# Kernel optimization log

Measured on AMD Instinct MI355X. Metric: run time of the kernel, lower is better.

## Reference

```python
import jax, jax.numpy as jnp
import numpy as np

H = 4            # num_attention_heads
EPS_LN = 1e-6    # LayerNorm eps
EPS_IN = 1e-5    # InstanceNorm2d eps (no affine)


def layer_norm(x, g, b):
    m = x.mean(-1, keepdims=True)
    v = ((x - m) ** 2).mean(-1, keepdims=True)
    return (x - m) * jax.lax.rsqrt(v + EPS_LN) * g + b


def instance_norm(s):
    # s: [B,H,C,KV]; InstanceNorm2d(H): normalize per (b,h) over spatial dims (C,KV)
    m = s.mean(axis=(2, 3), keepdims=True)
    v = s.var(axis=(2, 3), keepdims=True)
    return (s - m) * jax.lax.rsqrt(v + EPS_IN)


def _forward(emb1, emb2, emb3, emb4,
             an1_g, an1_b, Wq1, Wo1, fn1_g, fn1_b, fc11_w, fc11_b, fc12_w, fc12_b,
             an2_g, an2_b, Wq2, Wo2, fn2_g, fn2_b, fc21_w, fc21_b, fc22_w, fc22_b,
             an3_g, an3_b, Wq3, Wo3, fn3_g, fn3_b, fc31_w, fc31_b, fc32_w, fc32_b,
             an4_g, an4_b, Wq4, Wo4, fn4_g, fn4_b, fc41_w, fc41_b, fc42_w, fc42_b,
             anA_g, anA_b, Wk, Wv):
    embs = [emb1, emb2, emb3, emb4]
    branches = [
        (an1_g, an1_b, Wq1, Wo1, fn1_g, fn1_b, fc11_w, fc11_b, fc12_w, fc12_b),
        (an2_g, an2_b, Wq2, Wo2, fn2_g, fn2_b, fc21_w, fc21_b, fc22_w, fc22_b),
        (an3_g, an3_b, Wq3, Wo3, fn3_g, fn3_b, fc31_w, fc31_b, fc32_w, fc32_b),
        (an4_g, an4_b, Wq4, Wo4, fn4_g, fn4_b, fc41_w, fc41_b, fc42_w, fc42_b),
    ]
    emb_all = jnp.concatenate(embs, axis=-1)          # [B, n, KV]
    KV = emb_all.shape[-1]
    ea = layer_norm(emb_all, anA_g, anA_b)
    # per-head K/V projections (torch Linear: y = x @ W^T), stacked over heads
    K = jnp.einsum('bnk,hjk->bhnj', ea, Wk)           # [B,H,n,KV]
    V = jnp.einsum('bnk,hjk->bhnj', ea, Wv)           # [B,H,n,KV]
    scale = 1.0 / np.sqrt(KV).astype(np.float32)
    outs = []
    for e, (ag, ab, Wq, Wo, fg, fb, w1, b1, w2, b2) in zip(embs, branches):
        cx = layer_norm(e, ag, ab)                    # [B,n,C]
        Q = jnp.einsum('bnc,hdc->bhnd', cx, Wq)       # [B,H,n,C]
        # channel-attention scores: Q^T K over tokens -> [B,H,C,KV]
        scores = jnp.einsum('bhnd,bhnj->bhdj', Q, K) * scale
        probs = jax.nn.softmax(instance_norm(scores), axis=-1)
        # context [B,H,C,n] averaged over heads -> [B,n,C] (fused into einsum)
        ctx = jnp.einsum('bhdj,bhnj->bnd', probs, V) / H
        O = ctx @ Wo.T                                # out projection
        x = e + O                                     # residual
        h = layer_norm(x, fg, fb)
        h = jax.nn.gelu(h @ w1.T + b1, approximate=False)
        h = h @ w2.T + b2
        outs.append(x + h)                            # FFN residual
    return outs


def setup_inputs() -> dict:
    key = jax.random.key(0)
    B, N = 4, 784
    Cs = [64, 128, 256, 512]
    KV = sum(Cs)
    ks = iter(jax.random.split(key, 64))
    def nrm(shape, scale=0.02):
        return jax.random.normal(next(ks), shape, dtype=jnp.float32) * scale
    inp = {}
    for i, C in enumerate(Cs, 1):
        inp[f'emb{i}'] = jax.random.normal(next(ks), (B, N, C), dtype=jnp.float32)
        inp[f'an{i}_g'] = jnp.ones((C,), jnp.float32)
        inp[f'an{i}_b'] = jnp.zeros((C,), jnp.float32)
        inp[f'Wq{i}'] = nrm((H, C, C))
        inp[f'Wo{i}'] = nrm((C, C))
        inp[f'fn{i}_g'] = jnp.ones((C,), jnp.float32)
        inp[f'fn{i}_b'] = jnp.zeros((C,), jnp.float32)
        inp[f'fc{i}1_w'] = nrm((4 * C, C))
        inp[f'fc{i}1_b'] = nrm((4 * C,), 1e-6)
        inp[f'fc{i}2_w'] = nrm((C, 4 * C))
        inp[f'fc{i}2_b'] = nrm((C,), 1e-6)
    inp['anA_g'] = jnp.ones((KV,), jnp.float32)
    inp['anA_b'] = jnp.zeros((KV,), jnp.float32)
    inp['Wk'] = nrm((H, KV, KV))
    inp['Wv'] = nrm((H, KV, KV))
    return inp


def reference(emb1, emb2, emb3, emb4,
              an1_g, an1_b, Wq1, Wo1, fn1_g, fn1_b, fc11_w, fc11_b, fc12_w, fc12_b,
              an2_g, an2_b, Wq2, Wo2, fn2_g, fn2_b, fc21_w, fc21_b, fc22_w, fc22_b,
              an3_g, an3_b, Wq3, Wo3, fn3_g, fn3_b, fc31_w, fc31_b, fc32_w, fc32_b,
              an4_g, an4_b, Wq4, Wo4, fn4_g, fn4_b, fc41_w, fc41_b, fc42_w, fc42_b,
              anA_g, anA_b, Wk, Wv):
    outs = _forward(emb1, emb2, emb3, emb4,
                    an1_g, an1_b, Wq1, Wo1, fn1_g, fn1_b, fc11_w, fc11_b, fc12_w, fc12_b,
                    an2_g, an2_b, Wq2, Wo2, fn2_g, fn2_b, fc21_w, fc21_b, fc22_w, fc22_b,
                    an3_g, an3_b, Wq3, Wo3, fn3_g, fn3_b, fc31_w, fc31_b, fc32_w, fc32_b,
                    an4_g, an4_b, Wq4, Wo4, fn4_g, fn4_b, fc41_w, fc41_b, fc42_w, fc42_b,
                    anA_g, anA_b, Wk, Wv)
    return tuple(outs)
```

## Files before the change

### kernel.cpp

```cpp
#include <hip/hip_runtime.h>
#include <hip/hip_bf16.h>


using bf16 = __hip_bfloat16;
typedef __attribute__((ext_vector_type(8))) short short8;
typedef __attribute__((ext_vector_type(4))) float f32x4;

__device__ inline float bf2f(unsigned short u) {
    return __uint_as_float(((unsigned int)u) << 16);
}
__device__ inline unsigned short f2b(float f) {
    unsigned int u = __float_as_uint(f);
    return (unsigned short)((u + 0x7fffu + ((u >> 16) & 1u)) >> 16);
}
__device__ inline float ld1f(const float* p) { return *p; }
__device__ inline float ld1f(const bf16* p) { return bf2f(*(const unsigned short*)p); }
__device__ inline void st1(float* p, float v) { *p = v; }
__device__ inline void st1(bf16* p, float v) { *((unsigned short*)p) = f2b(v); }
__device__ inline float4 ld4f(const bf16* p) {
    ushort4 u = *(const ushort4*)p;
    return make_float4(bf2f(u.x), bf2f(u.y), bf2f(u.z), bf2f(u.w));
}

__device__ __forceinline__ void cp16(const void* g, void* l) {
    __builtin_amdgcn_global_load_lds(
        (const __attribute__((address_space(1))) void*)g,
        (__attribute__((address_space(3))) void*)l, 16, 0, 0);
}

__device__ inline float blockSum256(float v, float* red) {
    #pragma unroll
    for (int o = 32; o > 0; o >>= 1) v += __shfl_down(v, o);
    int t = threadIdx.x;
    if ((t & 63) == 0) red[t >> 6] = v;
    __syncthreads();
    float r = red[0] + red[1] + red[2] + red[3];
    __syncthreads();
    return r;
}
__device__ inline float blockMax256(float v, float* red) {
    #pragma unroll
    for (int o = 32; o > 0; o >>= 1) v = fmaxf(v, __shfl_down(v, o));
    int t = threadIdx.x;
    if ((t & 63) == 0) red[t >> 6] = v;
    __syncthreads();
    float r = fmaxf(fmaxf(red[0], red[1]), fmaxf(red[2], red[3]));
    __syncthreads();
    return r;
}

struct CvtN {
    const float* s[18];
    unsigned short* d[18];
    long n[18];
    float* z;
};
__global__ __launch_bounds__(256)
void cvtn_kernel(CvtN a) {
    if (a.z && blockIdx.x == 0 && threadIdx.x < 128) a.z[threadIdx.x] = 0.f;
    long tid = (long)blockIdx.x * 256 + threadIdx.x;
    long stride = (long)gridDim.x * 256;
    for (int g = 0; g < 18; g++) {
        const float* s = a.s[g];
        unsigned short* d = a.d[g];
        long n = a.n[g];
        for (long i = tid * 4; i < n; i += stride * 4) {
            float4 v = *(const float4*)(s + i);
            *(ushort4*)(d + i) = make_ushort4(f2b(v.x), f2b(v.y), f2b(v.z), f2b(v.w));
        }
    }
}

__global__ __launch_bounds__(512, 2)
void mfma8kv(const bf16* __restrict__ A, const bf16* __restrict__ B,
             bf16* __restrict__ KT, bf16* __restrict__ V) {
    __shared__ short Asl[2][2][256][32];
    __shared__ short Bsl[2][2][256][32];
    const int M = 3136, N = 7680, lda = 960, ldb = 960;
    int orig = (int)blockIdx.y * 32 + (int)blockIdx.x;
    int c = orig & 7, r2 = orig >> 3;
    int bx = (c & 3) * 8 + (r2 & 7);
    int by = (c >> 2) * 7 + (r2 >> 3);
    int m0 = by * 256, n0 = bx * 256;
    if (m0 >= M || n0 >= N) return;
    int t = threadIdx.x, lane = t & 63, wv = t >> 6;
    int col = lane & 15, quad = lane >> 4;
    int wm = wv >> 2, wn = wv & 3;
    f32x4 acc[8][4];
    #pragma unroll
    for (int i = 0; i < 8; i++)
        #pragma unroll
        for (int j = 0; j < 4; j++) acc[i][j] = (f32x4){0.f, 0.f, 0.f, 0.f};

    int srow = lane >> 2;
    int scol = ((lane & 3) ^ ((lane >> 3) & 3)) << 3;
    int rslot = (quad ^ ((col >> 1) & 3)) << 3;

    auto stageA = [&](int s2, int kt, int kh) {
        int k0 = kt * 64 + kh * 32;
        #pragma unroll
        for (int r = 0; r < 2; r++) {
            int R0 = (r * 8 + wv) * 16;
            cp16(A + (long)(m0 + R0 + srow) * lda + k0 + scol, &Asl[s2][kh][R0][0]);
        }
    };
    auto stageB = [&](int s2, int kt, int kh) {
        int k0 = kt * 64 + kh * 32;
        #pragma unroll
        for (int r = 0; r < 2; r++) {
            int R0 = (r * 8 + wv) * 16;
            cp16(B + (long)(n0 + R0 + srow) * ldb + k0 + scol, &Bsl[s2][kh][R0][0]);
        }
    };

    const int nk = 15;
    stageA(0, 0, 0); stageB(0, 0, 0); stageA(0, 0, 1); stageB(0, 0, 1);
    __syncthreads();

    for (int kt = 0; kt < nk; kt++) {
        int cur = kt & 1, nxt = cur ^ 1;
        bool st = (kt + 1 < nk);
        short8 af[8], bf8[4];
        #pragma unroll
        for (int ni = 0; ni < 4; ni++)
            bf8[ni] = *(const short8*)&Bsl[cur][0][wn * 64 + ni * 16 + col][rslot];
        #pragma unroll
        for (int mi = 0; mi < 4; mi++)
            af[mi] = *(const short8*)&Asl[cur][0][wm * 128 + mi * 16 + col][rslot];
        if (st) stageA(nxt, kt + 1, 0);
        __builtin_amdgcn_s_barrier();
        asm volatile("s_waitcnt lgkmcnt(0)" ::: "memory");
        __builtin_amdgcn_sched_barrier(0);
        __builtin_amdgcn_s_setprio(1);
        #pragma unroll
        for (int mi = 0; mi < 4; mi++)
            #pragma unroll
            for (int ni = 0; ni < 4; ni++)
// ... 185 lines not shown
            af[mi] = *(const short8*)&Asl[cur][wm * 64 + mi * 16 + col][rslot];
        #pragma unroll
        for (int ni = 0; ni < 4; ni++)
            bf4[ni] = *(const short8*)&Bsl[cur][wn * 64 + ni * 16 + col][rslot];
        int pend = 0;
        if (kt + 2 < nk) {
            int s3 = (kt + 2) % 3;
            stageA(s3, kt + 2); stageB(s3, kt + 2);
            if ((kt + 2) * 32 + 32 <= K) pend = (fA ? 2 : 0) + (fB ? 2 : 0);
        }
        __builtin_amdgcn_s_barrier();
        asm volatile("s_waitcnt lgkmcnt(0)" ::: "memory");
        __builtin_amdgcn_sched_barrier(0);
        __builtin_amdgcn_s_setprio(1);
        #pragma unroll
        for (int mi = 0; mi < 4; mi++)
            #pragma unroll
            for (int ni = 0; ni < 4; ni++)
                acc[mi][ni] = __builtin_amdgcn_mfma_f32_16x16x32_bf16(
                    af[mi], bf4[ni], acc[mi][ni], 0, 0, 0);
        __builtin_amdgcn_s_setprio(0);
        if (kt + 1 < nk) {
            if (pend == 4)      asm volatile("s_waitcnt vmcnt(4)" ::: "memory");
            else if (pend == 2) asm volatile("s_waitcnt vmcnt(2)" ::: "memory");
            else                asm volatile("s_waitcnt vmcnt(0)" ::: "memory");
            __builtin_amdgcn_s_barrier();
        }
    }
    float psum = 0.f, psq = 0.f;
    #pragma unroll
    for (int mi = 0; mi < 4; mi++) {
        int gmB = m0 + wm * 64 + mi * 16 + quad * 4;
        #pragma unroll
        for (int ni = 0; ni < 4; ni++) {
            int gn = n0 + wn * 64 + ni * 16 + col;
            if constexpr (TO) {
                if (gmB < M && gn < N) {
                    ushort4 w = make_ushort4(f2b(acc[mi][ni][0] * alpha),
                                             f2b(acc[mi][ni][1] * alpha),
                                             f2b(acc[mi][ni][2] * alpha),
                                             f2b(acc[mi][ni][3] * alpha));
                    *(ushort4*)((unsigned short*)Cp + (long)gn * ldc + gmB) = w;
                }
            } else {
                if (gn < N) {
                    float bz2 = bias ? bias[gn] : 0.f;
                    #pragma unroll
                    for (int r = 0; r < 4; r++) {
                        int gm = gmB + r;
                        if (gm < M) {
                            float v = acc[mi][ni][r] * alpha + bz2;
                            if (dogelu) v = 0.5f * v * (1.f + erff(v * 0.70710678118f));
                            if (res) v += ld1f(res + (long)gm * ldc + gn);
                            st1(Cp + (long)gm * ldc + gn, v);
                            psum += v; psq += v * v;
                        }
                    }
                }
            }
        }
    }
    if (stat) {
        __syncthreads();
        #pragma unroll
        for (int o = 32; o > 0; o >>= 1) {
            psum += __shfl_down(psum, o);
            psq  += __shfl_down(psq, o);
        }
        float* red = (float*)Asl;
        if ((t & 63) == 0) { red[wv] = psum; red[4 + wv] = psq; }
        __syncthreads();
        if (t == 0) {
            atomicAdd(&stat[2 * z],     red[0] + red[1] + red[2] + red[3]);
            atomicAdd(&stat[2 * z + 1], red[4] + red[5] + red[6] + red[7]);
        }
    }
}

struct G4 {
    const bf16* A[4]; const bf16* B[4]; void* Cv[4];
    const float* bias[4]; const void* res[4];
    int M[4], N[4], K[4], lda[4], ldb[4], ldc[4], nbx[4];
    int cum[5];
};
template <class CT, class RT>
__global__ __launch_bounds__(256, 3)
void mfma4g(G4 gp, int dogelu) {
    __shared__ short Asl[3][128][32];
    __shared__ short Bsl[3][128][32];
    int nwg = gridDim.x;
    int orig = blockIdx.x;
    int q = nwg >> 3, r8 = nwg & 7;
    int xcd = orig & 7, pos = orig >> 3;
    int wgid = (xcd < r8 ? xcd * (q + 1) : r8 * (q + 1) + (xcd - r8) * q) + pos;
    int gi = 0;
    if (wgid >= gp.cum[1]) gi = 1;
    if (wgid >= gp.cum[2]) gi = 2;
    if (wgid >= gp.cum[3]) gi = 3;
    int local = wgid - gp.cum[gi];
    int nbx = gp.nbx[gi];
    int by = local / nbx, bx = local - by * nbx;
    const bf16* A = gp.A[gi];
    const bf16* B = gp.B[gi];
    CT* Cp = (CT*)gp.Cv[gi];
    const float* bias = gp.bias[gi];
    const RT* res = (const RT*)gp.res[gi];
// ... 39 lines not shown
        int cur = kt % 3;
        short8 af[4], bf4[4];
        #pragma unroll
        for (int mi = 0; mi < 4; mi++)
            af[mi] = *(const short8*)&Asl[cur][wm * 64 + mi * 16 + col][rslot];
        #pragma unroll
        for (int ni = 0; ni < 4; ni++)
            bf4[ni] = *(const short8*)&Bsl[cur][wn * 64 + ni * 16 + col][rslot];
        bool st = (kt + 2 < nk);
        if (st) {
            int s3 = (kt + 2) % 3;
            stageA(s3, kt + 2); stageB(s3, kt + 2);
        }
        __builtin_amdgcn_s_barrier();
        asm volatile("s_waitcnt lgkmcnt(0)" ::: "memory");
        __builtin_amdgcn_sched_barrier(0);
        __builtin_amdgcn_s_setprio(1);
        #pragma unroll
        for (int mi = 0; mi < 4; mi++)
            #pragma unroll
            for (int ni = 0; ni < 4; ni++)
                acc[mi][ni] = __builtin_amdgcn_mfma_f32_16x16x32_bf16(
                    af[mi], bf4[ni], acc[mi][ni], 0, 0, 0);
        __builtin_amdgcn_s_setprio(0);
        if (kt + 1 < nk) {
            if (st) asm volatile("s_waitcnt vmcnt(4)" ::: "memory");
            else    asm volatile("s_waitcnt vmcnt(0)" ::: "memory");
            __builtin_amdgcn_s_barrier();
        }
    }
    #pragma unroll
    for (int mi = 0; mi < 4; mi++) {
        int gmB = m0 + wm * 64 + mi * 16 + quad * 4;
        #pragma unroll
        for (int ni = 0; ni < 4; ni++) {
            int gn = n0 + wn * 64 + ni * 16 + col;
            if (gn < N) {
                float bz2 = bias ? bias[gn] : 0.f;
                #pragma unroll
                for (int r = 0; r < 4; r++) {
                    int gm = gmB + r;
                    if (gm < M) {
                        float v = acc[mi][ni][r] + bz2;
                        if (dogelu) v = 0.5f * v * (1.f + erff(v * 0.70710678118f));
                        if (res) v += ld1f(res + (long)gm * ldc + gn);
                        st1(Cp + (long)gm * ldc + gn, v);
                    }
                }
            }
        }
    }
}

template <int TM, int TN, class CT, class RT, bool TO>
__global__ __launch_bounds__(256)
void mfma2(const bf16* __restrict__ A, long Ah, long Ab, int lda,
           const bf16* __restrict__ B, long Bh, long Bb, int ldb,
           CT* __restrict__ Cp, long Ch, long Cb, int ldc,
           const float* __restrict__ bias, const RT* __restrict__ res,
           int M, int N, int K, float alpha, int dogelu,
           float* __restrict__ stat) {
    constexpr int MI = TM / 32, NI = TN / 32;
    __shared__ short As[2][TM * 32];
    __shared__ short Bs[2][TN * 32];
    int z = blockIdx.z;
    A += (long)(z & 3) * Ah + (long)(z >> 2) * Ab;
    B += (long)(z & 3) * Bh + (long)(z >> 2) * Bb;
    Cp += (long)(z & 3) * Ch + (long)(z >> 2) * Cb;
    int m0 = blockIdx.y * TM, n0 = blockIdx.x * TN;
    int t = threadIdx.x, lane = t & 63, wv = t >> 6;
    int col = lane & 15, quad = lane >> 4;
    int wm = wv >> 1, wn = wv & 1;
    f32x4 acc[MI][NI];
    #pragma unroll
    for (int i = 0; i < MI; i++)
        #pragma unroll
        for (int j = 0; j < NI; j++) acc[i][j] = (f32x4){0.f, 0.f, 0.f, 0.f};

    const bool fastblk = (m0 + TM <= M) && (n0 + TN <= N);
    int lrow = lane >> 2;
    int lcol = ((lane & 3) ^ ((lane >> 3) & 3)) << 3;
    int sr = t >> 2;
    int swz = ((t & 3) ^ ((t >> 3) & 3)) << 3;
    int sdst = (t & 3) << 3;
    int rdslot = (quad ^ ((col >> 1) & 3)) << 3;

    auto stage = [&](int b, int k0) {
        if (fastblk && (k0 + 32 <= K)) {
            #pragma unroll
            for (int u = 0; u < TM / 64; u++) {
                int c = wv + 4 * u;
                int r = c * 16 + lrow;
                cp16(A + (long)(m0 + r) * lda + k0 + lcol, &As[b][c * 512]);
            }
            #pragma unroll
            for (int u = 0; u < TN / 64; u++) {
                int c = wv + 4 * u;
                int r = c * 16 + lrow;
                cp16(B + (long)(n0 + r) * ldb + k0 + lcol, &Bs[b][c * 512]);
            }
        } else {
            #pragma unroll
            for (int u = 0; u < TM / 64; u++) {
                int r = sr + u * 64;
                float4 v = make_float4(0.f, 0.f, 0.f, 0.f);
                if (m0 + r < M && k0 + swz < K)
                    v = *(const float4*)(A + (long)(m0 + r) * lda + k0 + swz);
                *(float4*)&As[b][r * 32 + sdst] = v;
            }
            #pragma unroll
            for (int u = 0; u < TN / 64; u++) {
                int r = sr + u * 64;
                float4 v = make_float4(0.f, 0.f, 0.f, 0.f);
                if (n0 + r < N && k0 + swz < K)
                    v = *(const float4*)(B + (long)(n0 + r) * ldb + k0 + swz);
                *(float4*)&Bs[b][r * 32 + sdst] = v;
            }
        }
    };

    int nk = (K + 31) >> 5;
    stage(0, 0);
    __syncthreads();
    int cur = 0;
    for (int s = 0; s < nk; s++) {
        if (s + 1 < nk) stage(cur ^ 1, (s + 1) * 32);
        short8 af[MI], bfr[NI];
        #pragma unroll
        for (int mi = 0; mi < MI; mi++)
            af[mi] = *(const short8*)&As[cur][(wm * (TM / 2) + mi * 16 + col) * 32 + rdslot];
        #pragma unroll
        for (int ni = 0; ni < NI; ni++)
            bfr[ni] = *(const short8*)&Bs[cur][(wn * (TN / 2) + ni * 16 + col) * 32 + rdslot];
        #pragma unroll
        for (int mi = 0; mi < MI; mi++)
            #pragma unroll
            for (int ni = 0; ni < NI; ni++)
                acc[mi][ni] = __builtin_amdgcn_mfma_f32_16x16x32_bf16(
                    af[mi], bfr[ni], acc[mi][ni], 0, 0, 0);
        if (s + 1 < nk) __syncthreads();
        cur ^= 1;
    }
    float psum = 0.f, psq = 0.f;
    #pragma unroll
    for (int mi = 0; mi < MI; mi++) {
        int gmB = m0 + wm * (TM / 2) + mi * 16 + quad * 4;
        #pragma unroll
        for (int ni = 0; ni < NI; ni++) {
            int gn = n0 + wn * (TN / 2) + ni * 16 + col;
            if constexpr (TO) {
                if (gmB < M && gn < N) {
                    ushort4 w = make_ushort4(f2b(acc[mi][ni][0] * alpha),
                                             f2b(acc[mi][ni][1] * alpha),
                                             f2b(acc[mi][ni][2] * alpha),
                                             f2b(acc[mi][ni][3] * alpha));
                    *(ushort4*)((unsigned short*)Cp + (long)gn * ldc + gmB) = w;
                }
            } else {
                if (gn < N) {
                    float bz = bias ? bias[gn] : 0.f;
                    #pragma unroll
                    for (int r = 0; r < 4; r++) {
                        int gm = gmB + r;
                        if (gm < M) {
                            float v = acc[mi][ni][r] * alpha + bz;
                            if (dogelu) v = 0.5f * v * (1.f + erff(v * 0.70710678118f));
                            if (res) v += ld1f(res + (long)gm * ldc + gn);
                            st1(Cp + (long)gm * ldc + gn, v);
                            psum += v; psq += v * v;
                        }
                    }
                }
            }
        }
    }
    if (stat) {
        __syncthreads();
        #pragma unroll
        for (int o = 32; o > 0; o >>= 1) {
            psum += __shfl_down(psum, o);
            psq  += __shfl_down(psq, o);
        }
        float* red = (float*)As;
        if ((t & 63) == 0) { red[wv] = psum; red[4 + wv] = psq; }
        __syncthreads();
        if (t == 0) {
            atomicAdd(&stat[2 * z],     red[0] + red[1] + red[2] + red[3]);
            atomicAdd(&stat[2 * z + 1], red[4] + red[5] + red[6] + red[7]);
        }
    }
}

struct LNA {
    const float* e[4];
    const float* ag[4];
    const float* ab[4];
    const float* cg;
    const float* cbb;
    bf16* y[4];
    bf16* ea;
};
__global__ __launch_bounds__(256)
void ln_all_kernel(LNA a) {
    __shared__ float x[960];
    __shared__ float red[4];
    long row = blockIdx.x;
    int t = threadIdx.x;
    const int off[5] = {0, 64, 192, 448, 960};
    {
        const float* p1 = a.e[0] + row * 64;
        const float* p2 = a.e[1] + row * 128;
        const float* p3 = a.e[2] + row * 256;
        const float* p4 = a.e[3] + row * 512;
        if (t < 64) x[t] = p1[t];
        for (int i = t; i < 128; i += 256) x[64 + i]  = p2[i];
        for (int i = t; i < 256; i += 256) x[192 + i] = p3[i];
        for (int i = t; i < 512; i += 256) x[448 + i] = p4[i];
    }
    __syncthreads();
    float ssum[4], ssq[4];
    #pragma unroll
    for (int br = 0; br < 4; br++) {
        float s = 0.f, q = 0.f;
        for (int i = off[br] + t; i < off[br + 1]; i += 256) {
            float v = x[i]; s += v; q += v * v;
        }
        ssum[br] = blockSum256(s, red);
        ssq[br]  = blockSum256(q, red);
    }
    float S1 = ssum[0] + ssum[1] + ssum[2] + ssum[3];
    float S2 = ssq[0] + ssq[1] + ssq[2] + ssq[3];
    float muA = S1 * (1.f / 960.f);
    float rA = rsqrtf(S2 * (1.f / 960.f) - muA * muA + 1e-6f);
    for (int i = t; i < 960; i += 256)
        st1(a.ea + row * 960 + i, (x[i] - muA) * rA * a.cg[i] + a.cbb[i]);
    #pragma unroll
    for (int br = 0; br < 4; br++) {
        int C = off[br + 1] - off[br];
        float mu = ssum[br] / C;
        float rr = rsqrtf(ssq[br] / C - mu * mu + 1e-6f);
        const float* g = a.ag[br];
        const float* b = a.ab[br];
        bf16* y = a.y[br] + row * C;
        for (int i = t; i < C; i += 256)
            st1(y + i, (x[off[br] + i] - mu) * rr * g[i] + b[i]);
    }
}

struct LR4 {
    const bf16* X[4];
    const float* g[4];
    const float* b[4];
    bf16* Y[4];
    int C[4];
};
__global__ __launch_bounds__(256)
void ln_rows4_kernel(LR4 a) {
    __shared__ float x[512];
    __shared__ float red[4];
    int br = blockIdx.y;
    long row = blockIdx.x;
    int C = a.C[br];
    int t = threadIdx.x;
    const bf16* xr = a.X[br] + row * C;
    float s = 0.f, q = 0.f;
    for (int i = t; i < C; i += 256) { float v = ld1f(xr + i); x[i] = v; s += v; q += v * v; }
    float S1 = blockSum256(s, red), S2 = blockSum256(q, red);
    float mu = S1 / C;
    float r = rsqrtf(S2 / C - mu * mu + 1e-6f);
    const float* g = a.g[br];
    const float* b = a.b[br];
    bf16* y = a.Y[br] + row * C;
    for (int i = t; i < C; i += 256)
        st1(y + i, (x[i] - mu) * r * g[i] + b[i]);
}

__global__ __launch_bounds__(256)
void ctx_sum_kernel(const bf16* __restrict__ tmp, bf16* __restrict__ ctx, long NTC) {
    long i = ((long)blockIdx.x * 256 + threadIdx.x) * 4;
    float4 a = ld4f(tmp + i);
    float4 b = ld4f(tmp + NTC + i);
    float4 c = ld4f(tmp + 2 * NTC + i);
    float4 d = ld4f(tmp + 3 * NTC + i);
    ushort4 o = make_ushort4(f2b((a.x + b.x + c.x + d.x) * 0.25f),
                             f2b((a.y + b.y + c.y + d.y) * 0.25f),
                             f2b((a.z + b.z + c.z + d.z) * 0.25f),
                             f2b((a.w + b.w + c.w + d.w) * 0.25f));
    *(ushort4*)(ctx + i) = o;
}

__global__ __launch_bounds__(256)
void softmax_kernel(bf16* __restrict__ S, const float* __restrict__ stat, int C) {
    __shared__ float x[960];
    __shared__ float red[4];
    long r = blockIdx.x;
    int t = threadIdx.x;
    int z = (int)(r / C);
    int d = (int)(r % C);
    float n = 960.f * (float)C;
    float s0 = stat[2 * z], q0 = stat[2 * z + 1];
    float mu = s0 / n;
    float rs = rsqrtf(q0 / n - mu * mu + 1e-5f);
    int h = z & 3, b = z >> 2;
    bf16* row = S + (long)b * C * 3840 + (long)d * 3840 + h * 960;
    float mx = -3.4e38f;
    for (int i = t; i < 960; i += 256) {
        float v = ld1f(row + i) * rs; x[i] = v; mx = fmaxf(mx, v);
    }
    float M = blockMax256(mx, red);
    float s = 0.f;
    for (int i = t; i < 960; i += 256) { float e = __expf(x[i] - M); x[i] = e; s += e; }
    float Ssum = blockSum256(s, red);
    float inv = 1.f / Ssum;
    for (int i = t; i < 960; i += 256) st1(row + i, x[i] * inv);
}

extern "C" void kernel_launch(void* const* d_in, const int* in_sizes, int n_in,
                              void* d_out, int out_size, void* d_ws, size_t ws_size,
                              hipStream_t stream) {
    (void)in_sizes; (void)n_in; (void)out_size; (void)ws_size;
    const int Cs[4] = {64, 128, 256, 512};
    const float *emb[4], *ang[4], *anb[4], *Wq[4], *Wo[4], *fng[4], *fnb[4], *w1[4], *b1[4], *w2[4], *b2[4];
    for (int i = 0; i < 4; i++) {
        const int base = i * 11;
        emb[i] = (const float*)d_in[base + 0];
        ang[i] = (const float*)d_in[base + 1];
        anb[i] = (const float*)d_in[base + 2];
        Wq[i]  = (const float*)d_in[base + 3];
        Wo[i]  = (const float*)d_in[base + 4];
        fng[i] = (const float*)d_in[base + 5];
        fnb[i] = (const float*)d_in[base + 6];
        w1[i]  = (const float*)d_in[base + 7];
        b1[i]  = (const float*)d_in[base + 8];
        w2[i]  = (const float*)d_in[base + 9];
        b2[i]  = (const float*)d_in[base + 10];
    }
    const float* anAg = (const float*)d_in[44];
    const float* anAb = (const float*)d_in[45];
    const float* Wk   = (const float*)d_in[46];
    const float* Wv   = (const float*)d_in[47];

    const int NT = 3136;
    char* wsb = (char*)d_ws;
    unsigned short* wp = (unsigned short*)(wsb);
    float* statb = (float*)(wsb + 9052160);
    bf16*  KT    = (bf16*)(wsb + 9053184);
    bf16*  hid   = (bf16*)(wsb + 9053184);
    bf16*  Vb2   = (bf16*)(wsb + 33137664);
    bf16*  xball = (bf16*)(wsb + 33137664);
    bf16*  cx3   = (bf16*)(wsb + 39158784);
    bf16*  QT    = (bf16*)(wsb + 57222144);
    bf16*  wkv   = (bf16*)(wsb + 57222144);
    bf16*  Sb    = (bf16*)(wsb + 70067200);
    bf16*  ea    = (bf16*)(wsb + 71967744);
    bf16*  cxall = (bf16*)(wsb + 85795840);
    bf16*  cx2   = (bf16*)(wsb + 91816960);

    const long wb[4] = {0, 53248, 266240, 1118208};
    const long co[4] = {0, 64L * NT, 192L * NT, 448L * NT};
    const long ho[4] = {0, 802816, 2408448, 5619712};

    float* out = (float*)d_out;
    const long ooff[4] = {0, 200704, 602112, 1404928};
    const float scale = 0.03227486121f;

    {
        CvtN a;
        a.s[0] = Wk; a.d[0] = (unsigned short*)wkv;           a.n[0] = 3686400;
        a.s[1] = Wv; a.d[1] = (unsigned short*)wkv + 3686400; a.n[1] = 3686400;
        for (int i = 0; i < 4; i++) {
            const long C2 = (long)Cs[i] * Cs[i];
            a.s[2 + 4 * i] = Wq[i]; a.d[2 + 4 * i] = wp + wb[i];          a.n[2 + 4 * i] = 4 * C2;
            a.s[3 + 4 * i] = Wo[i]; a.d[3 + 4 * i] = wp + wb[i] + 4 * C2; a.n[3 + 4 * i] = C2;
            a.s[4 + 4 * i] = w1[i]; a.d[4 + 4 * i] = wp + wb[i] + 5 * C2; a.n[4 + 4 * i] = 4 * C2;
            a.s[5 + 4 * i] = w2[i]; a.d[5 + 4 * i] = wp + wb[i] + 9 * C2; a.n[5 + 4 * i] = 4 * C2;
        }
        a.z = statb;
        cvtn_kernel<<<1024, 256, 0, stream>>>(a);
    }
    {
        LNA a;
        for (int i = 0; i < 4; i++) {
            a.e[i] = emb[i]; a.ag[i] = ang[i]; a.ab[i] = anb[i];
            a.y[i] = cxall + co[i];
        }
        a.cg = anAg; a.cbb = anAb; a.ea = ea;
        ln_all_kernel<<<3136, 256, 0, stream>>>(a);
    }
    mfma8kv<<<dim3(32, 14, 1), 512, 0, stream>>>(ea, wkv, KT, Vb2);

    for (int i = 0; i < 4; i++) {
        const int C = Cs[i];
        const long C2 = (long)C * C;
        bf16* wqb = (bf16*)(wp + wb[i]);
        float* st = statb + 32 * i;
        if (C >= 128) {
            mfma4<bf16, float, true><<<dim3(C / 128, 26, 4), 256, 0, stream>>>(
                cxall + co[i], 0, 0, C, wqb, C2, 0, C, QT, (long)C * NT, 0, NT,
                nullptr, (const float*)nullptr, NT, C, C, 3328, C, 0, 0,
                1.f, 0, nullptr);
            mfma4<bf16, float, false><<<dim3(8, C / 128, 16), 256, 0, stream>>>(
                QT, (long)C * NT, 784, NT, KT, 3010560, 784, NT,
                Sb, 960, (long)C * 3840, 3840,
                nullptr, (const float*)nullptr, C, 960, 784, C, 1024, 0, 0,
                scale, 0, st);
        } else {
            mfma2<64, 64, bf16, float, true><<<dim3(1, 49, 4), 256, 0, stream>>>(
                cxall + co[i], 0, 0, C, wqb, C2, 0, C, QT, (long)C * NT, 0, NT,
                nullptr, (const float*)nullptr, NT, C, C, 1.f, 0, nullptr);
            mfma2<64, 64, bf16, float, false><<<dim3(15, 1, 16), 256, 0, stream>>>(
                QT, (long)C * NT, 784, NT, KT, 3010560, 784, NT,
                Sb, 960, (long)C * 3840, 3840,
                nullptr, (const float*)nullptr, C, 960, 784, scale, 0, st);
        }
        softmax_kernel<<<16 * C, 256, 0, stream>>>(Sb, st, C);
        if (C >= 128)
            mfma4<bf16, float, false><<<dim3(C / 128, 7, 16), 256, 0, stream>>>(
                Vb2, 960, 784L * 3840, 3840, Sb, 960, (long)C * 3840, 3840,
                QT, (long)NT * C, 784L * C, C,
                nullptr, (const float*)nullptr, 784, C, 960, 896, C, 0, 0,
                1.f, 0, nullptr);
        else
            mfma2<64, 64, bf16, float, false><<<dim3(1, 13, 16), 256, 0, stream>>>(
                Vb2, 960, 784L * 3840, 3840, Sb, 960, (long)C * 3840, 3840,
                QT, (long)NT * C, 784L * C, C,
                nullptr, (const float*)nullptr, 784, C, 960, 1.f, 0, nullptr);
        ctx_sum_kernel<<<(int)(((long)NT * C) / 1024), 256, 0, stream>>>(
            QT, cx2 + co[i], (long)NT * C);
    }

    {
        G4 g;
        int cum = 0;
        for (int i = 0; i < 4; i++) {
            const int C = Cs[i];
            const long C2 = (long)C * C;
            g.A[i] = cx2 + co[i]; g.B[i] = (const bf16*)(wp + wb[i] + 4 * C2);
            g.Cv[i] = xball + co[i];
            g.bias[i] = nullptr; g.res[i] = emb[i];
            g.M[i] = NT; g.N[i] = C; g.K[i] = C;
            g.lda[i] = C; g.ldb[i] = C; g.ldc[i] = C;
            g.nbx[i] = (C >= 128) ? C / 128 : 1;
            g.cum[i] = cum; cum += g.nbx[i] * 26;
        }
        g.cum[4] = cum;
        mfma4g<bf16, float><<<cum, 256, 0, stream>>>(g, 0);
    }
    {
        LR4 a;
        for (int i = 0; i < 4; i++) {
            a.X[i] = xball + co[i]; a.g[i] = fng[i]; a.b[i] = fnb[i];
            a.Y[i] = cx3 + co[i]; a.C[i] = Cs[i];
        }
        ln_rows4_kernel<<<dim3(3136, 4), 256, 0, stream>>>(a);
    }
    {
        G4 g;
        int cum = 0;
        for (int i = 0; i < 4; i++) {
            const int C = Cs[i];
            const long C2 = (long)C * C;
            g.A[i] = cx3 + co[i]; g.B[i] = (const bf16*)(wp + wb[i] + 5 * C2);
            g.Cv[i] = hid + ho[i];
            g.bias[i] = b1[i]; g.res[i] = nullptr;
            g.M[i] = NT; g.N[i] = 4 * C; g.K[i] = C;
            g.lda[i] = C; g.ldb[i] = C; g.ldc[i] = 4 * C;
            g.nbx[i] = 4 * C / 128;
            g.cum[i] = cum; cum += g.nbx[i] * 26;
        }
        g.cum[4] = cum;
        mfma4g<bf16, float><<<cum, 256, 0, stream>>>(g, 1);
    }
    {
        G4 g;
        int cum = 0;
        for (int i = 0; i < 4; i++) {
            const int C = Cs[i];
            const long C2 = (long)C * C;
            g.A[i] = hid + ho[i]; g.B[i] = (const bf16*)(wp + wb[i] + 9 * C2);
            g.Cv[i] = out + ooff[i];
            g.bias[i] = b2[i]; g.res[i] = xball + co[i];
            g.M[i] = NT; g.N[i] = C; g.K[i] = 4 * C;
            g.lda[i] = 4 * C; g.ldb[i] = 4 * C; g.ldc[i] = C;
            g.nbx[i] = (C >= 128) ? C / 128 : 1;
            g.cum[i] = cum; cum += g.nbx[i] * 26;
        }
        g.cum[4] = cum;
        mfma4g<float, bf16><<<cum, 256, 0, stream>>>(g, 0);
    }
}
```

Baseline: 721.5 us.

## Batch per-branch attention GEMMs and softmax into grouped multi-problem launches

Replaces the per-branch loop of Q-projection, score GEMM, softmax, PV GEMM and ctx-sum launches with grouped kernels that handle all branches in one launch each. A new grouped 128x128 GEMM kernel (mfmaGZ) uses a triple-buffered LDS pipeline and XCD-aware workgroup remapping, with separate workspace regions per branch so the branches can run concurrently. The largest branch keeps its dedicated Q and score GEMMs, while the others are grouped. The goal is to cut launch overhead and poor occupancy from small-C branches, at the cost of more workspace aliasing and more complex indexing.

```diff
diff --git a/kernel.cpp b/kernel.cpp
--- a/kernel.cpp
+++ b/kernel.cpp
@@ -76,13 +76,13 @@
              bf16* __restrict__ KT, bf16* __restrict__ V) {
     __shared__ short Asl[2][2][256][32];
     __shared__ short Bsl[2][2][256][32];
-    const int M = 3136, N = 7680, lda = 960, ldb = 960;
+    const int M = 3136, lda = 960, ldb = 960;
     int orig = (int)blockIdx.y * 32 + (int)blockIdx.x;
     int c = orig & 7, r2 = orig >> 3;
     int bx = (c & 3) * 8 + (r2 & 7);
     int by = (c >> 2) * 7 + (r2 >> 3);
     int m0 = by * 256, n0 = bx * 256;
-    if (m0 >= M || n0 >= N) return;
+    if (m0 >= M || n0 >= 7680) return;
     int t = threadIdx.x, lane = t & 63, wv = t >> 6;
     int col = lane & 15, quad = lane >> 4;
     int wm = wv >> 2, wn = wv & 3;
@@ -374,6 +374,188 @@
                             float v = acc[mi][ni][r] * alpha + bz2;
                             if (dogelu) v = 0.5f * v * (1.f + erff(v * 0.70710678118f));
                             if (res) v += ld1f(res + (long)gm * ldc + gn);
+                            st1(Cp + (long)gm * ldc + gn, v);
+                            psum += v; psq += v * v;
+                        }
+                    }
+                }
+            }
+        }
+    }
+    if (stat) {
+        __syncthreads();
+        #pragma unroll
+        for (int o = 32; o > 0; o >>= 1) {
+            psum += __shfl_down(psum, o);
+            psq  += __shfl_down(psq, o);
+        }
+        float* red = (float*)Asl;
+        if ((t & 63) == 0) { red[wv] = psum; red[4 + wv] = psq; }
+        __syncthreads();
+        if (t == 0) {
+            atomicAdd(&stat[2 * z],     red[0] + red[1] + red[2] + red[3]);
+            atomicAdd(&stat[2 * z + 1], red[4] + red[5] + red[6] + red[7]);
+        }
+    }
+}
+
+struct GZ {
+    const bf16* A[4]; const bf16* B[4]; bf16* C[4];
+    long Ah[4], Ab[4], Bh[4], Bb[4], Ch[4], Cb[4];
+    int lda[4], ldb[4], ldc[4], M[4], N[4], K[4], Mpad[4], Npad[4], nbx[4], nby[4];
+    float alpha[4];
+    float* stat[4];
+    int cum[5];
+};
+template <bool TO>
+__global__ __launch_bounds__(256, 3)
+void mfmaGZ(GZ g) {
+    __shared__ short Asl[3][128][32];
+    __shared__ short Bsl[3][128][32];
+    int nwg = gridDim.x;
+    int orig = blockIdx.x;
+    int q = nwg >> 3, r8 = nwg & 7;
+    int xcd = orig & 7, pos = orig >> 3;
+    int wgid = (xcd < r8 ? xcd * (q + 1) : r8 * (q + 1) + (xcd - r8) * q) + pos;
+    int gi = 0;
+    if (wgid >= g.cum[1]) gi = 1;
+    if (wgid >= g.cum[2]) gi = 2;
+    if (wgid >= g.cum[3]) gi = 3;
+    int local = wgid - g.cum[gi];
+    int nbx = g.nbx[gi], nby = g.nby[gi];
+    int z = local / (nbx * nby);
+    int rem = local - z * nbx * nby;
+    int by = rem / nbx, bx = rem - by * nbx;
+    const bf16* A = g.A[gi] + (long)(z & 3) * g.Ah[gi] + (long)(z >> 2) * g.Ab[gi];
+    const bf16* B = g.B[gi] + (long)(z & 3) * g.Bh[gi] + (long)(z >> 2) * g.Bb[gi];
+    bf16* Cp = g.C[gi] + (long)(z & 3) * g.Ch[gi] + (long)(z >> 2) * g.Cb[gi];
+    int lda = g.lda[gi], ldb = g.ldb[gi], ldc = g.ldc[gi];
+    int M = g.M[gi], N = g.N[gi], K = g.K[gi];
+    int Mpad = g.Mpad[gi], Npad = g.Npad[gi];
+    float alpha = g.alpha[gi];
+    float* stat = g.stat[gi];
+
+    int m0 = by * 128, n0 = bx * 128;
+    int t = threadIdx.x, lane = t & 63, wv = t >> 6;
+    int col = lane & 15, quad = lane >> 4;
+    int wm = wv >> 1, wn = wv & 1;
+    f32x4 acc[4][4];
+    #pragma unroll
+    for (int i = 0; i < 4; i++)
+        #pragma unroll
+        for (int j = 0; j < 4; j++) acc[i][j] = (f32x4){0.f, 0.f, 0.f, 0.f};
+
+    const bool fA = (m0 + 128 <= Mpad);
+    const bool fB = (n0 + 128 <= Npad);
+    int srow = lane >> 2;
+    int scol = ((lane & 3) ^ ((lane >> 3) & 3)) << 3;
+    int rslot = (quad ^ ((col >> 1) & 3)) << 3;
+
+    auto stageA = [&](int s3, int kt) {
+        int k0 = kt * 32;
+        if (fA && k0 + 32 <= K) {
+            #pragma unroll
+            for (int r = 0; r < 2; r++) {
+                int R0 = (r * 4 + wv) * 16;
+                cp16(A + (long)(m0 + R0 + srow) * lda + k0 + scol, &Asl[s3][R0][0]);
+            }
+        } else {
+            #pragma unroll
+            for (int r = 0; r < 2; r++) {
+                int idx = r * 256 + t;
+                int row = idx >> 2, sl = idx & 3;
+                int f2 = (row >> 1) & 3;
+                short8 v = {};
+                if (m0 + row < M && k0 + sl * 8 < K)
+                    v = *(const short8*)(A + (long)(m0 + row) * lda + k0 + sl * 8);
+                *(short8*)&Asl[s3][row][(sl ^ f2) * 8] = v;
+            }
+            asm volatile("s_waitcnt lgkmcnt(0)" ::: "memory");
+        }
+    };
+    auto stageB = [&](int s3, int kt) {
+        int k0 = kt * 32;
+        if (fB && k0 + 32 <= K) {
+            #pragma unroll
+            for (int r = 0; r < 2; r++) {
+                int R0 = (r * 4 + wv) * 16;
+                cp16(B + (long)(n0 + R0 + srow) * ldb + k0 + scol, &Bsl[s3][R0][0]);
+            }
+        } else {
+            #pragma unroll
+            for (int r = 0; r < 2; r++) {
+                int idx = r * 256 + t;
+                int row = idx >> 2, sl = idx & 3;
+                int f2 = (row >> 1) & 3;
+                short8 v = {};
+                if (n0 + row < N && k0 + sl * 8 < K)
+                    v = *(const short8*)(B + (long)(n0 + row) * ldb + k0 + sl * 8);
+                *(short8*)&Bsl[s3][row][(sl ^ f2) * 8] = v;
+            }
+            asm volatile("s_waitcnt lgkmcnt(0)" ::: "memory");
+        }
+    };
+
+    int nk = (K + 31) >> 5;
+    stageA(0, 0); stageB(0, 0);
+    stageA(1, 1); stageB(1, 1);
+    __syncthreads();
+
+    for (int kt = 0; kt < nk; kt++) {
+        int cur = kt % 3;
+        short8 af[4], bf4[4];
+        #pragma unroll
+        for (int mi = 0; mi < 4; mi++)
+            af[mi] = *(const short8*)&Asl[cur][wm * 64 + mi * 16 + col][rslot];
+        #pragma unroll
+        for (int ni = 0; ni < 4; ni++)
+            bf4[ni] = *(const short8*)&Bsl[cur][wn * 64 + ni * 16 + col][rslot];
+        int pend = 0;
+        if (kt + 2 < nk) {
+            int s3 = (kt + 2) % 3;
+            stageA(s3, kt + 2); stageB(s3, kt + 2);
+            if ((kt + 2) * 32 + 32 <= K) pend = (fA ? 2 : 0) + (fB ? 2 : 0);
+        }
+        __builtin_amdgcn_s_barrier();
+        asm volatile("s_waitcnt lgkmcnt(0)" ::: "memory");
+        __builtin_amdgcn_sched_barrier(0);
+        __builtin_amdgcn_s_setprio(1);
+        #pragma unroll
+        for (int mi = 0; mi < 4; mi++)
+            #pragma unroll
+            for (int ni = 0; ni < 4; ni++)
+                acc[mi][ni] = __builtin_amdgcn_mfma_f32_16x16x32_bf16(
+                    af[mi], bf4[ni], acc[mi][ni], 0, 0, 0);
+        __builtin_amdgcn_s_setprio(0);
+        if (kt + 1 < nk) {
+            if (pend == 4)      asm volatile("s_waitcnt vmcnt(4)" ::: "memory");
+            else if (pend == 2) asm volatile("s_waitcnt vmcnt(2)" ::: "memory");
+            else                asm volatile("s_waitcnt vmcnt(0)" ::: "memory");
+            __builtin_amdgcn_s_barrier();
+        }
+    }
+    float psum = 0.f, psq = 0.f;
+    #pragma unroll
+    for (int mi = 0; mi < 4; mi++) {
+        int gmB = m0 + wm * 64 + mi * 16 + quad * 4;
+        #pragma unroll
+        for (int ni = 0; ni < 4; ni++) {
+            int gn = n0 + wn * 64 + ni * 16 + col;
+            if constexpr (TO) {
+                if (gmB < M && gn < N) {
+                    ushort4 w = make_ushort4(f2b(acc[mi][ni][0] * alpha),
+                                             f2b(acc[mi][ni][1] * alpha),
+                                             f2b(acc[mi][ni][2] * alpha),
+                                             f2b(acc[mi][ni][3] * alpha));
+                    *(ushort4*)((unsigned short*)Cp + (long)gn * ldc + gmB) = w;
+                }
+            } else {
+                if (gn < N) {
+                    #pragma unroll
+                    for (int r = 0; r < 4; r++) {
+                        int gm = gmB + r;
+                        if (gm < M) {
+                            float v = acc[mi][ni][r] * alpha;
                             st1(Cp + (long)gm * ldc + gn, v);
                             psum += v; psq += v * v;
                         }
@@ -519,145 +701,6 @@
     }
 }
 
-template <int TM, int TN, class CT, class RT, bool TO>
-__global__ __launch_bounds__(256)
-void mfma2(const bf16* __restrict__ A, long Ah, long Ab, int lda,
-           const bf16* __restrict__ B, long Bh, long Bb, int ldb,
-           CT* __restrict__ Cp, long Ch, long Cb, int ldc,
-           const float* __restrict__ bias, const RT* __restrict__ res,
-           int M, int N, int K, float alpha, int dogelu,
-           float* __restrict__ stat) {
-    constexpr int MI = TM / 32, NI = TN / 32;
-    __shared__ short As[2][TM * 32];
-    __shared__ short Bs[2][TN * 32];
-    int z = blockIdx.z;
-    A += (long)(z & 3) * Ah + (long)(z >> 2) * Ab;
-    B += (long)(z & 3) * Bh + (long)(z >> 2) * Bb;
-    Cp += (long)(z & 3) * Ch + (long)(z >> 2) * Cb;
-    int m0 = blockIdx.y * TM, n0 = blockIdx.x * TN;
-    int t = threadIdx.x, lane = t & 63, wv = t >> 6;
-    int col = lane & 15, quad = lane >> 4;
-    int wm = wv >> 1, wn = wv & 1;
-    f32x4 acc[MI][NI];
-    #pragma unroll
-    for (int i = 0; i < MI; i++)
-        #pragma unroll
-        for (int j = 0; j < NI; j++) acc[i][j] = (f32x4){0.f, 0.f, 0.f, 0.f};
-
-    const bool fastblk = (m0 + TM <= M) && (n0 + TN <= N);
-    int lrow = lane >> 2;
-    int lcol = ((lane & 3) ^ ((lane >> 3) & 3)) << 3;
-    int sr = t >> 2;
-    int swz = ((t & 3) ^ ((t >> 3) & 3)) << 3;
-    int sdst = (t & 3) << 3;
-    int rdslot = (quad ^ ((col >> 1) & 3)) << 3;
-
-    auto stage = [&](int b, int k0) {
-        if (fastblk && (k0 + 32 <= K)) {
-            #pragma unroll
-            for (int u = 0; u < TM / 64; u++) {
-                int c = wv + 4 * u;
-                int r = c * 16 + lrow;
-                cp16(A + (long)(m0 + r) * lda + k0 + lcol, &As[b][c * 512]);
-            }
-            #pragma unroll
-            for (int u = 0; u < TN / 64; u++) {
-                int c = wv + 4 * u;
-                int r = c * 16 + lrow;
-                cp16(B + (long)(n0 + r) * ldb + k0 + lcol, &Bs[b][c * 512]);
-            }
-        } else {
-            #pragma unroll
-            for (int u = 0; u < TM / 64; u++) {
-                int r = sr + u * 64;
-                float4 v = make_float4(0.f, 0.f, 0.f, 0.f);
-                if (m0 + r < M && k0 + swz < K)
-                    v = *(const float4*)(A + (long)(m0 + r) * lda + k0 + swz);
-                *(float4*)&As[b][r * 32 + sdst] = v;
-            }
-            #pragma unroll
-            for (int u = 0; u < TN / 64; u++) {
-                int r = sr + u * 64;
-                float4 v = make_float4(0.f, 0.f, 0.f, 0.f);
-                if (n0 + r < N && k0 + swz < K)
-                    v = *(const float4*)(B + (long)(n0 + r) * ldb + k0 + swz);
-                *(float4*)&Bs[b][r * 32 + sdst] = v;
-            }
-        }
-    };
-
-    int nk = (K + 31) >> 5;
-    stage(0, 0);
-    __syncthreads();
-    int cur = 0;
-    for (int s = 0; s < nk; s++) {
-        if (s + 1 < nk) stage(cur ^ 1, (s + 1) * 32);
-        short8 af[MI], bfr[NI];
-        #pragma unroll
-        for (int mi = 0; mi < MI; mi++)
-            af[mi] = *(const short8*)&As[cur][(wm * (TM / 2) + mi * 16 + col) * 32 + rdslot];
-        #pragma unroll
-        for (int ni = 0; ni < NI; ni++)
-            bfr[ni] = *(const short8*)&Bs[cur][(wn * (TN / 2) + ni * 16 + col) * 32 + rdslot];
-        #pragma unroll
-        for (int mi = 0; mi < MI; mi++)
-            #pragma unroll
-            for (int ni = 0; ni < NI; ni++)
-                acc[mi][ni] = __builtin_amdgcn_mfma_f32_16x16x32_bf16(
-                    af[mi], bfr[ni], acc[mi][ni], 0, 0, 0);
-        if (s + 1 < nk) __syncthreads();
-        cur ^= 1;
-    }
-    float psum = 0.f, psq = 0.f;
-    #pragma unroll
-    for (int mi = 0; mi < MI; mi++) {
-        int gmB = m0 + wm * (TM / 2) + mi * 16 + quad * 4;
-        #pragma unroll
-        for (int ni = 0; ni < NI; ni++) {
-            int gn = n0 + wn * (TN / 2) + ni * 16 + col;
-            if constexpr (TO) {
-                if (gmB < M && gn < N) {
-                    ushort4 w = make_ushort4(f2b(acc[mi][ni][0] * alpha),
-                                             f2b(acc[mi][ni][1] * alpha),
-                                             f2b(acc[mi][ni][2] * alpha),
-                                             f2b(acc[mi][ni][3] * alpha));
-                    *(ushort4*)((unsigned short*)Cp + (long)gn * ldc + gmB) = w;
-                }
-            } else {
-                if (gn < N) {
-                    float bz = bias ? bias[gn] : 0.f;
-                    #pragma unroll
-                    for (int r = 0; r < 4; r++) {
-                        int gm = gmB + r;
-                        if (gm < M) {
-                            float v = acc[mi][ni][r] * alpha + bz;
-                            if (dogelu) v = 0.5f * v * (1.f + erff(v * 0.70710678118f));
-                            if (res) v += ld1f(res + (long)gm * ldc + gn);
-                            st1(Cp + (long)gm * ldc + gn, v);
-                            psum += v; psq += v * v;
-                        }
-                    }
-                }
-            }
-        }
-    }
-    if (stat) {
-        __syncthreads();
-        #pragma unroll
-        for (int o = 32; o > 0; o >>= 1) {
-            psum += __shfl_down(psum, o);
-            psq  += __shfl_down(psq, o);
-        }
-        float* red = (float*)As;
-        if ((t & 63) == 0) { red[wv] = psum; red[4 + wv] = psq; }
-        __syncthreads();
-        if (t == 0) {
-            atomicAdd(&stat[2 * z],     red[0] + red[1] + red[2] + red[3]);
-            atomicAdd(&stat[2 * z + 1], red[4] + red[5] + red[6] + red[7]);
-        }
-    }
-}
-
 struct LNA {
     const float* e[4];
     const float* ag[4];
@@ -742,34 +785,32 @@
         st1(y + i, (x[i] - mu) * r * g[i] + b[i]);
 }
 
+struct SMX {
+    bf16* S[4];
+    const float* stat[4];
+    int C[4];
+    int cum[5];
+};
 __global__ __launch_bounds__(256)
-void ctx_sum_kernel(const bf16* __restrict__ tmp, bf16* __restrict__ ctx, long NTC) {
-    long i = ((long)blockIdx.x * 256 + threadIdx.x) * 4;
-    float4 a = ld4f(tmp + i);
-    float4 b = ld4f(tmp + NTC + i);
-    float4 c = ld4f(tmp + 2 * NTC + i);
-    float4 d = ld4f(tmp + 3 * NTC + i);
-    ushort4 o = make_ushort4(f2b((a.x + b.x + c.x + d.x) * 0.25f),
-                             f2b((a.y + b.y + c.y + d.y) * 0.25f),
-                             f2b((a.z + b.z + c.z + d.z) * 0.25f),
-                             f2b((a.w + b.w + c.w + d.w) * 0.25f));
-    *(ushort4*)(ctx + i) = o;
-}
-
-__global__ __launch_bounds__(256)
-void softmax_kernel(bf16* __restrict__ S, const float* __restrict__ stat, int C) {
+void softmax_all_kernel(SMX a) {
     __shared__ float x[960];
     __shared__ float red[4];
-    long r = blockIdx.x;
+    int rid = blockIdx.x;
+    int gi = 0;
+    if (rid >= a.cum[1]) gi = 1;
+    if (rid >= a.cum[2]) gi = 2;
+    if (rid >= a.cum[3]) gi = 3;
+    int local = rid - a.cum[gi];
+    int C = a.C[gi];
+    int z = local / C;
+    int d = local - z * C;
     int t = threadIdx.x;
-    int z = (int)(r / C);
-    int d = (int)(r % C);
     float n = 960.f * (float)C;
-    float s0 = stat[2 * z], q0 = stat[2 * z + 1];
+    float s0 = a.stat[gi][2 * z], q0 = a.stat[gi][2 * z + 1];
     float mu = s0 / n;
     float rs = rsqrtf(q0 / n - mu * mu + 1e-5f);
     int h = z & 3, b = z >> 2;
-    bf16* row = S + (long)b * C * 3840 + (long)d * 3840 + h * 960;
+    bf16* row = a.S[gi] + (long)b * C * 3840 + (long)d * 3840 + h * 960;
     float mx = -3.4e38f;
     for (int i = t; i < 960; i += 256) {
         float v = ld1f(row + i) * rs; x[i] = v; mx = fmaxf(mx, v);
@@ -780,6 +821,34 @@
     float Ssum = blockSum256(s, red);
     float inv = 1.f / Ssum;
     for (int i = t; i < 960; i += 256) st1(row + i, x[i] * inv);
+}
+
+struct CSX {
+    const bf16* tmp[4];
+    bf16* ctx[4];
+    long NTC[4];
+    int cum[5];
+};
+__global__ __launch_bounds__(256)
+void ctxsum_all_kernel(CSX a) {
+    int bid = blockIdx.x;
+    int gi = 0;
+    if (bid >= a.cum[1]) gi = 1;
+    if (bid >= a.cum[2]) gi = 2;
+    if (bid >= a.cum[3]) gi = 3;
+    long local = bid - a.cum[gi];
+    long NTC = a.NTC[gi];
+    const bf16* tmp = a.tmp[gi];
+    long i = (local * 256 + threadIdx.x) * 4;
+    float4 p = ld4f(tmp + i);
+    float4 b = ld4f(tmp + NTC + i);
+    float4 c = ld4f(tmp + 2 * NTC + i);
+    float4 d = ld4f(tmp + 3 * NTC + i);
+    ushort4 o = make_ushort4(f2b((p.x + b.x + c.x + d.x) * 0.25f),
+                             f2b((p.y + b.y + c.y + d.y) * 0.25f),
+                             f2b((p.z + b.z + c.z + d.z) * 0.25f),
+                             f2b((p.w + b.w + c.w + d.w) * 0.25f));
+    *(ushort4*)(a.ctx[gi] + i) = o;
 }
 
 extern "C" void kernel_launch(void* const* d_in, const int* in_sizes, int n_in,
@@ -812,23 +881,27 @@
     unsigned short* wp = (unsigned short*)(wsb);
     float* statb = (float*)(wsb + 9052160);
     bf16*  KT    = (bf16*)(wsb + 9053184);
-    bf16*  hid   = (bf16*)(wsb + 9053184);
+    bf16*  tmpb  = KT;
+    bf16*  hid   = KT;
     bf16*  Vb2   = (bf16*)(wsb + 33137664);
-    bf16*  xball = (bf16*)(wsb + 33137664);
-    bf16*  cx3   = (bf16*)(wsb + 39158784);
-    bf16*  QT    = (bf16*)(wsb + 57222144);
+    bf16*  cx2   = (bf16*)(wsb + 33137664);
+    bf16*  xball = (bf16*)(wsb + 39158784);
+    bf16*  cx3   = (bf16*)(wsb + 45179904);
+    bf16*  QTp   = (bf16*)(wsb + 57222144);
     bf16*  wkv   = (bf16*)(wsb + 57222144);
-    bf16*  Sb    = (bf16*)(wsb + 70067200);
+    bf16*  S5    = (bf16*)(wsb + 70067200);
     bf16*  ea    = (bf16*)(wsb + 71967744);
+    bf16*  SR    = (bf16*)(wsb + 85795840);
     bf16*  cxall = (bf16*)(wsb + 85795840);
-    bf16*  cx2   = (bf16*)(wsb + 91816960);
-
-    const long wb[4] = {0, 53248, 266240, 1118208};
-    const long co[4] = {0, 64L * NT, 192L * NT, 448L * NT};
-    const long ho[4] = {0, 802816, 2408448, 5619712};
+
+    const long wb[4]  = {0, 53248, 266240, 1118208};
+    const long co[4]  = {0, 200704, 602112, 1404928};
+    const long ho[4]  = {0, 802816, 2408448, 5619712};
+    const long qro[3] = {4816896, 3211264, 0};
+    const long sro[3] = {5898240, 3932160, 0};
+    const long tpo[4] = {11239424, 9633792, 6422528, 0};
 
     float* out = (float*)d_out;
-    const long ooff[4] = {0, 200704, 602112, 1404928};
     const float scale = 0.03227486121f;
 
     {
@@ -856,46 +929,98 @@
     }
     mfma8kv<<<dim3(32, 14, 1), 512, 0, stream>>>(ea, wkv, KT, Vb2);
 
-    for (int i = 0; i < 4; i++) {
-        const int C = Cs[i];
-        const long C2 = (long)C * C;
-        bf16* wqb = (bf16*)(wp + wb[i]);
-        float* st = statb + 32 * i;
-        if (C >= 128) {
-            mfma4<bf16, float, true><<<dim3(C / 128, 26, 4), 256, 0, stream>>>(
-                cxall + co[i], 0, 0, C, wqb, C2, 0, C, QT, (long)C * NT, 0, NT,
-                nullptr, (const float*)nullptr, NT, C, C, 3328, C, 0, 0,
-                1.f, 0, nullptr);
-            mfma4<bf16, float, false><<<dim3(8, C / 128, 16), 256, 0, stream>>>(
-                QT, (long)C * NT, 784, NT, KT, 3010560, 784, NT,
-                Sb, 960, (long)C * 3840, 3840,
-                nullptr, (const float*)nullptr, C, 960, 784, C, 1024, 0, 0,
-                scale, 0, st);
-        } else {
-            mfma2<64, 64, bf16, float, true><<<dim3(1, 49, 4), 256, 0, stream>>>(
-                cxall + co[i], 0, 0, C, wqb, C2, 0, C, QT, (long)C * NT, 0, NT,
-                nullptr, (const float*)nullptr, NT, C, C, 1.f, 0, nullptr);
-            mfma2<64, 64, bf16, float, false><<<dim3(15, 1, 16), 256, 0, stream>>>(
-                QT, (long)C * NT, 784, NT, KT, 3010560, 784, NT,
-                Sb, 960, (long)C * 3840, 3840,
-                nullptr, (const float*)nullptr, C, 960, 784, scale, 0, st);
-        }
-        softmax_kernel<<<16 * C, 256, 0, stream>>>(Sb, st, C);
-        if (C >= 128)
-            mfma4<bf16, float, false><<<dim3(C / 128, 7, 16), 256, 0, stream>>>(
-                Vb2, 960, 784L * 3840, 3840, Sb, 960, (long)C * 3840, 3840,
-                QT, (long)NT * C, 784L * C, C,
-                nullptr, (const float*)nullptr, 784, C, 960, 896, C, 0, 0,
-                1.f, 0, nullptr);
-        else
-            mfma2<64, 64, bf16, float, false><<<dim3(1, 13, 16), 256, 0, stream>>>(
-                Vb2, 960, 784L * 3840, 3840, Sb, 960, (long)C * 3840, 3840,
-                QT, (long)NT * C, 784L * C, C,
-                nullptr, (const float*)nullptr, 784, C, 960, 1.f, 0, nullptr);
-        ctx_sum_kernel<<<(int)(((long)NT * C) / 1024), 256, 0, stream>>>(
-            QT, cx2 + co[i], (long)NT * C);
-    }
-
+    mfma4<bf16, float, true><<<dim3(4, 26, 4), 256, 0, stream>>>(
+        cxall + co[3], 0, 0, 512, (const bf16*)(wp + wb[3]), 262144, 0, 512,
+        QTp, 512L * NT, 0, NT,
+        nullptr, (const float*)nullptr, NT, 512, 512, 3328, 512, 0, 0,
+        1.f, 0, nullptr);
+    mfma4<bf16, float, false><<<dim3(8, 4, 16), 256, 0, stream>>>(
+        QTp, 512L * NT, 784, NT, KT, 3010560, 784, NT,
+        S5, 960, 512L * 3840, 3840,
+        nullptr, (const float*)nullptr, 512, 960, 784, 512, 1024, 0, 0,
+        scale, 0, statb + 32 * 3);
+    {
+        GZ g;
+        int cum = 0;
+        const int ord[3] = {2, 1, 0};
+        for (int j = 0; j < 3; j++) {
+            int i = ord[j], C = Cs[i];
+            g.A[j] = cxall + co[i]; g.Ah[j] = 0; g.Ab[j] = 0; g.lda[j] = C;
+            g.B[j] = (const bf16*)(wp + wb[i]); g.Bh[j] = (long)C * C; g.Bb[j] = 0; g.ldb[j] = C;
+            g.C[j] = QTp + qro[i]; g.Ch[j] = (long)C * NT; g.Cb[j] = 0; g.ldc[j] = NT;
+            g.M[j] = NT; g.N[j] = C; g.K[j] = C;
+            g.Mpad[j] = 3328; g.Npad[j] = (C >= 128) ? C : 64;
+            g.nbx[j] = (C >= 128) ? C / 128 : 1; g.nby[j] = 26;
+            g.alpha[j] = 1.f; g.stat[j] = nullptr;
+            g.cum[j] = cum; cum += g.nbx[j] * 26 * 4;
+        }
+        g.cum[3] = cum; g.cum[4] = cum;
+        mfmaGZ<true><<<cum, 256, 0, stream>>>(g);
+    }
+    {
+        GZ g;
+        int cum = 0;
+        const int ord[3] = {2, 1, 0};
+        for (int j = 0; j < 3; j++) {
+            int i = ord[j], C = Cs[i];
+            g.A[j] = QTp + qro[i]; g.Ah[j] = (long)C * NT; g.Ab[j] = 784; g.lda[j] = NT;
+            g.B[j] = KT; g.Bh[j] = 3010560; g.Bb[j] = 784; g.ldb[j] = NT;
+            g.C[j] = SR + sro[i]; g.Ch[j] = 960; g.Cb[j] = (long)C * 3840; g.ldc[j] = 3840;
+            g.M[j] = C; g.N[j] = 960; g.K[j] = 784;
+            g.Mpad[j] = (C >= 128) ? C : 64; g.Npad[j] = 1024;
+            g.nbx[j] = 8; g.nby[j] = (C >= 128) ? C / 128 : 1;
+            g.alpha[j] = scale; g.stat[j] = statb + 32 * i;
+            g.cum[j] = cum; cum += 8 * g.nby[j] * 16;
+        }
+        g.cum[3] = cum; g.cum[4] = cum;
+        mfmaGZ<false><<<cum, 256, 0, stream>>>(g);
+    }
+    {
+        SMX a;
+        const int ord[4] = {3, 2, 1, 0};
+        int cum = 0;
+        for (int j = 0; j < 4; j++) {
+            int i = ord[j], C = Cs[i];
+            a.S[j] = (i == 3) ? S5 : SR + sro[i];
+            a.stat[j] = statb + 32 * i;
+            a.C[j] = C;
+            a.cum[j] = cum; cum += 16 * C;
+        }
+        a.cum[4] = cum;
+        softmax_all_kernel<<<cum, 256, 0, stream>>>(a);
+    }
+    {
+        GZ g;
+        int cum = 0;
+        const int ord[4] = {3, 2, 1, 0};
+        for (int j = 0; j < 4; j++) {
+            int i = ord[j], C = Cs[i];
+            g.A[j] = Vb2; g.Ah[j] = 960; g.Ab[j] = 784L * 3840; g.lda[j] = 3840;
+            g.B[j] = (i == 3) ? S5 : SR + sro[i];
+            g.Bh[j] = 960; g.Bb[j] = (long)C * 3840; g.ldb[j] = 3840;
+            g.C[j] = tmpb + tpo[i]; g.Ch[j] = (long)NT * C; g.Cb[j] = 784L * C; g.ldc[j] = C;
+            g.M[j] = 784; g.N[j] = C; g.K[j] = 960;
+            g.Mpad[j] = 896; g.Npad[j] = (C >= 128) ? C : 64;
+            g.nbx[j] = (C >= 128) ? C / 128 : 1; g.nby[j] = 7;
+            g.alpha[j] = 1.f; g.stat[j] = nullptr;
+            g.cum[j] = cum; cum += g.nbx[j] * 7 * 16;
+        }
+        g.cum[4] = cum;
+        mfmaGZ<false><<<cum, 256, 0, stream>>>(g);
+    }
+    {
+        CSX a;
+        int cum = 0;
+        const int ord[4] = {3, 2, 1, 0};
+        for (int j = 0; j < 4; j++) {
+            int i = ord[j], C = Cs[i];
+            a.tmp[j] = tmpb + tpo[i]; a.ctx[j] = cx2 + co[i];
+            a.NTC[j] = (long)NT * C;
+            a.cum[j] = cum; cum += (int)(((long)NT * C) / 1024);
+        }
+        a.cum[4] = cum;
+        ctxsum_all_kernel<<<cum, 256, 0, stream>>>(a);
+    }
     {
         G4 g;
         int cum = 0;
@@ -945,7 +1070,7 @@
             const int C = Cs[i];
             const long C2 = (long)C * C;
             g.A[i] = hid + ho[i]; g.B[i] = (const bf16*)(wp + wb[i] + 9 * C2);
-            g.Cv[i] = out + ooff[i];
+            g.Cv[i] = out + co[i];
             g.bias[i] = b2[i]; g.res[i] = xball + co[i];
             g.M[i] = NT; g.N[i] = C; g.K[i] = 4 * C;
             g.lda[i] = 4 * C; g.ldb[i] = 4 * C; g.ldc[i] = C;
```

Result: faster. 632.3 us (-12.4%).
